# Kernel tuning notes

Measured on AMD Instinct MI355X. Metric: run time of the kernel, lower is better.

The kernel has to match this reference:

```python
import jax, jax.numpy as jnp
import numpy as np

B, C, R, Cc = 16384, 30, 7, 7

def setup_inputs() -> dict:
    key = jax.random.key(0)
    k1, k2, k3 = jax.random.split(key, 3)
    pred = jax.random.uniform(k1, (B, C, R, Cc), dtype=jnp.float32)
    label = jax.random.uniform(k2, (B, C, R, Cc), dtype=jnp.float32)
    obj = (jax.random.uniform(k3, (B, R, Cc)) > 0.7).astype(jnp.float32)
    label = label.at[:, 4].set(obj)
    return {"pred": pred, "label": label}

def _boxes(t, cols, rows, nrow, ncol, off):
    # t: [b,30,r,c]; channels off..off+3 are (x,y,w,h) relative to cell
    x, y, w, h = t[:, off], t[:, off + 1], t[:, off + 2], t[:, off + 3]
    cx = (x + cols) / ncol
    cy = (y + rows) / nrow
    return cx - w / 2, cy - h / 2, cx + w / 2, cy + h / 2

def _iou(a, b):
    ax1, ay1, ax2, ay2 = a
    bx1, by1, bx2, by2 = b
    iw = jnp.maximum(jnp.minimum(ax2, bx2) - jnp.maximum(ax1, bx1), 0.0)
    ih = jnp.maximum(jnp.minimum(ay2, by2) - jnp.maximum(ay1, by1), 0.0)
    inter = iw * ih
    area_a = (ax2 - ax1) * (ay2 - ay1)
    area_b = (bx2 - bx1) * (by2 - by1)
    return inter / (area_a + area_b - inter + 1e-10)

def reference(pred, label):
    b_size = pred.shape[0]
    nrow, ncol = pred.shape[-2], pred.shape[-1]
    cols = jnp.arange(ncol, dtype=pred.dtype)[None, None, :]  # [1,1,c]
    rows = jnp.arange(nrow, dtype=pred.dtype)[None, :, None]  # [1,r,1]

    bbox1 = _boxes(pred, cols, rows, nrow, ncol, 0)
    bbox2 = _boxes(pred, cols, rows, nrow, ncol, 5)
    lbox = _boxes(label, cols, rows, nrow, ncol, 0)
    iou1 = _iou(bbox1, lbox)  # [b,r,c]
    iou2 = _iou(bbox2, lbox)
    choose1 = iou1 >= iou2

    # coord loss candidates (sum over the 2 xy channels / 2 wh channels)
    coord1 = 5.0 * jnp.sum((pred[:, 0:2] - label[:, 0:2]) ** 2, axis=1) \
           + jnp.sum((jnp.sqrt(pred[:, 2:4]) - jnp.sqrt(label[:, 2:4])) ** 2, axis=1)
    coord2 = 5.0 * jnp.sum((pred[:, 5:7] - label[:, 5:7]) ** 2, axis=1) \
           + jnp.sum((jnp.sqrt(pred[:, 7:9]) - jnp.sqrt(label[:, 7:9])) ** 2, axis=1)

    obj1 = (pred[:, 4] - iou1) ** 2
    obj2 = (pred[:, 9] - iou2) ** 2

    coord = jnp.where(choose1, coord1, coord2)
    obj_conf = jnp.where(choose1, obj1, obj2)
    noobj_conf_obj = 0.5 * jnp.where(choose1, obj2, obj1)
    class_l = jnp.sum((pred[:, 10:] - label[:, 10:]) ** 2, axis=1)

    obj_cell = coord + obj_conf + noobj_conf_obj + class_l
    # note: original sums the two confidences THEN squares (faithful to source)
    noobj_cell = 0.5 * (pred[:, 4] + pred[:, 9]) ** 2

    is_obj = label[:, 4] == 1.0
    per_cell = jnp.where(is_obj, obj_cell, noobj_cell)
    return jnp.sum(per_cell) / b_size
```

## Files before the change

### kernel.cpp

```cpp
#include <hip/hip_runtime.h>


typedef float v2f __attribute__((ext_vector_type(2)));

#define NBATCH 16384
#define RECF 1470
#define BLOCK 256
#define GRID 2048
#define NWAVES (GRID * 4)

__device__ __forceinline__ float sq(float x) { return x * x; }

__device__ __forceinline__ float block_reduce(float v, float* smem, int tid) {
#pragma unroll
    for (int off = 32; off > 0; off >>= 1) v += __shfl_down(v, off, 64);
    const int lane = tid & 63, wave = tid >> 6;
    if (lane == 0) smem[wave] = v;
    __syncthreads();
    return smem[0] + smem[1] + smem[2] + smem[3];
}

__global__ __launch_bounds__(BLOCK) void k_class(const float* __restrict__ pred,
                                                 const float* __restrict__ label,
                                                 float* __restrict__ partials) {
    __shared__ float smem[4];
    const int tid = threadIdx.x, lane = tid & 63, wv = tid >> 6;
    const int gw = blockIdx.x * 4 + wv;
    const int c0 = (2 * lane) % 49;
    float acc = 0.0f;

    for (int rec = gw; rec < NBATCH; rec += NWAVES) {
        const float* rp = pred + (size_t)rec * RECF;
        const float* rl = label + (size_t)rec * RECF;
        float w49 = (lane < 49) ? rl[196 + lane] : 0.0f;
        int c = c0;
#pragma unroll
        for (int it = 0; it < 8; ++it) {
            int k = it * 64 + lane;
            v2f p2 = {0.0f, 0.0f}, l2 = {0.0f, 0.0f};
            if (k < 490) {
                p2 = __builtin_nontemporal_load((const v2f*)(rp + 490 + 2 * k));
                l2 = __builtin_nontemporal_load((const v2f*)(rl + 490 + 2 * k));
            }
            float w0 = __shfl(w49, c, 64);
            int cn = (c == 48) ? 0 : c + 1;
            float w1 = __shfl(w49, cn, 64);
            float d0 = p2.x - l2.x, d1 = p2.y - l2.y;
            acc += w0 * d0 * d0 + w1 * d1 * d1;
            c += 30; if (c >= 49) c -= 49;
        }
    }

    float s = block_reduce(acc, smem, tid);
    if (tid == 0) partials[blockIdx.x] = s;
}

__global__ __launch_bounds__(BLOCK) void k_box(const float* __restrict__ pred,
                                               const float* __restrict__ label,
                                               float* __restrict__ partials) {
    __shared__ float lds[4][960];
    __shared__ float smem[4];
    const int tid = threadIdx.x, lane = tid & 63, wv = tid >> 6;
    const int gw = blockIdx.x * 4 + wv;
    float* ldsw = &lds[wv][0];
    v2f* wp2 = (v2f*)ldsw;
    v2f* wl2 = (v2f*)(ldsw + 496);

    const int rr = lane / 7, cc = lane - rr * 7;
    const float fr = (float)rr, fcl = (float)cc;
    const float inv7 = 1.0f / 7.0f;
    float acc = 0.0f;

    for (int rec = gw; rec < NBATCH; rec += NWAVES) {
        const v2f* gp = (const v2f*)(pred + (size_t)rec * RECF);
        const v2f* gl = (const v2f*)(label + (size_t)rec * RECF);
#pragma unroll
        for (int r4 = 0; r4 < 4; ++r4) {
            int idx = r4 * 64 + lane;
            if (idx < 245) wp2[idx] = __builtin_nontemporal_load(gp + idx);
            if (idx < 221) wl2[idx] = __builtin_nontemporal_load(gl + idx);
        }
        asm volatile("s_waitcnt lgkmcnt(0)" ::: "memory");

        if (lane < 49) {
            float p[10], l[9];
#pragma unroll
            for (int ch = 0; ch < 10; ++ch) p[ch] = ldsw[ch * 49 + lane];
#pragma unroll
            for (int ch = 0; ch < 9; ++ch) l[ch] = ldsw[496 + ch * 49 + lane];

            float lcx = (l[0] + fcl) * inv7;
            float lcy = (l[1] + fr) * inv7;
            float lhw = l[2] * 0.5f, lhh = l[3] * 0.5f;
            float lx1 = lcx - lhw, ly1 = lcy - lhh;
            float lx2 = lcx + lhw, ly2 = lcy + lhh;
            float larea = (lx2 - lx1) * (ly2 - ly1);

            float cx1 = (p[0] + fcl) * inv7, cy1 = (p[1] + fr) * inv7;
            float x11 = cx1 - p[2] * 0.5f, y11 = cy1 - p[3] * 0.5f;
            float x12 = cx1 + p[2] * 0.5f, y12 = cy1 + p[3] * 0.5f;
            float iw1 = fmaxf(fminf(x12, lx2) - fmaxf(x11, lx1), 0.0f);
            float ih1 = fmaxf(fminf(y12, ly2) - fmaxf(y11, ly1), 0.0f);
            float int1 = iw1 * ih1;
            float a1 = (x12 - x11) * (y12 - y11);
            float iou1 = int1 / (a1 + larea - int1 + 1e-10f);

            float cx2 = (p[5] + fcl) * inv7, cy2 = (p[6] + fr) * inv7;
            float x21 = cx2 - p[7] * 0.5f, y21 = cy2 - p[8] * 0.5f;
            float x22 = cx2 + p[7] * 0.5f, y22 = cy2 + p[8] * 0.5f;
            float iw2 = fmaxf(fminf(x22, lx2) - fmaxf(x21, lx1), 0.0f);
            float ih2 = fmaxf(fminf(y22, ly2) - fmaxf(y21, ly1), 0.0f);
            float int2 = iw2 * ih2;
            float a2 = (x22 - x21) * (y22 - y21);
            float iou2 = int2 / (a2 + larea - int2 + 1e-10f);

            bool ch1 = iou1 >= iou2;

            float coord1 = 5.0f * (sq(p[0] - l[0]) + sq(p[1] - l[1]))
                         + sq(sqrtf(p[2]) - sqrtf(l[2])) + sq(sqrtf(p[3]) - sqrtf(l[3]));
            float coord2 = 5.0f * (sq(p[5] - l[5]) + sq(p[6] - l[6]))
                         + sq(sqrtf(p[7]) - sqrtf(l[7])) + sq(sqrtf(p[8]) - sqrtf(l[8]));
            float obj1 = sq(p[4] - iou1);
            float obj2 = sq(p[9] - iou2);

            float obj_cell = (ch1 ? coord1 : coord2)
                           + (ch1 ? obj1 : obj2)
                           + 0.5f * (ch1 ? obj2 : obj1);
            float noobj_cell = 0.5f * sq(p[4] + p[9]);

            acc += (l[4] == 1.0f) ? obj_cell : noobj_cell;
        }
    }

    float s = block_reduce(acc, smem, tid);
    if (tid == 0) partials[blockIdx.x] = s;
}

__global__ __launch_bounds__(BLOCK) void k_reduce(const float* __restrict__ partials,
                                                  float* __restrict__ out) {
    __shared__ float smem[4];
    float s = 0.0f;
#pragma unroll
    for (int it = 0; it < 2 * GRID / BLOCK; ++it)
        s += partials[it * BLOCK + threadIdx.x];
    float t = block_reduce(s, smem, threadIdx.x);
    if (threadIdx.x == 0) out[0] = t * (1.0f / (float)NBATCH);
}

extern "C" void kernel_launch(void* const* d_in, const int* in_sizes, int n_in,
                              void* d_out, int out_size, void* d_ws, size_t ws_size,
                              hipStream_t stream) {
    const float* pred  = (const float*)d_in[0];
    const float* label = (const float*)d_in[1];
    float* out = (float*)d_out;
    float* part1 = (float*)d_ws;
    float* part2 = part1 + GRID;

    k_class<<<GRID, BLOCK, 0, stream>>>(pred, label, part1);
    k_box<<<GRID, BLOCK, 0, stream>>>(pred, label, part2);
    k_reduce<<<1, BLOCK, 0, stream>>>(part1, out);
}
```

Baseline: 203.3 us.

## Fuse class and box kernels into one wave-per-record kernel

Merges the class-loss kernel and the box/IoU kernel into one kernel where each wave handles exactly one record. All global loads for the record are issued up front into registers, then the box channels are staged to LDS while the class loss is computed. This removes one kernel launch and the grid-stride loops, and lets both parts overlap their memory traffic. In exchange it raises register pressure from holding 24 vector loads per lane, launches many more blocks, and drops the nontemporal load hints.

```diff
diff --git a/kernel.cpp b/kernel.cpp
--- a/kernel.cpp
+++ b/kernel.cpp
@@ -6,8 +6,7 @@
 #define NBATCH 16384
 #define RECF 1470
 #define BLOCK 256
-#define GRID 2048
-#define NWAVES (GRID * 4)
+#define GRID (NBATCH / 4)
 
 __device__ __forceinline__ float sq(float x) { return x * x; }
 
@@ -20,116 +19,112 @@
     return smem[0] + smem[1] + smem[2] + smem[3];
 }
 
-__global__ __launch_bounds__(BLOCK) void k_class(const float* __restrict__ pred,
+__global__ __launch_bounds__(BLOCK) void k_fused(const float* __restrict__ pred,
                                                  const float* __restrict__ label,
                                                  float* __restrict__ partials) {
-    __shared__ float smem[4];
-    const int tid = threadIdx.x, lane = tid & 63, wv = tid >> 6;
-    const int gw = blockIdx.x * 4 + wv;
-    const int c0 = (2 * lane) % 49;
-    float acc = 0.0f;
-
-    for (int rec = gw; rec < NBATCH; rec += NWAVES) {
-        const float* rp = pred + (size_t)rec * RECF;
-        const float* rl = label + (size_t)rec * RECF;
-        float w49 = (lane < 49) ? rl[196 + lane] : 0.0f;
-        int c = c0;
-#pragma unroll
-        for (int it = 0; it < 8; ++it) {
-            int k = it * 64 + lane;
-            v2f p2 = {0.0f, 0.0f}, l2 = {0.0f, 0.0f};
-            if (k < 490) {
-                p2 = __builtin_nontemporal_load((const v2f*)(rp + 490 + 2 * k));
-                l2 = __builtin_nontemporal_load((const v2f*)(rl + 490 + 2 * k));
-            }
-            float w0 = __shfl(w49, c, 64);
-            int cn = (c == 48) ? 0 : c + 1;
-            float w1 = __shfl(w49, cn, 64);
-            float d0 = p2.x - l2.x, d1 = p2.y - l2.y;
-            acc += w0 * d0 * d0 + w1 * d1 * d1;
-            c += 30; if (c >= 49) c -= 49;
-        }
-    }
-
-    float s = block_reduce(acc, smem, tid);
-    if (tid == 0) partials[blockIdx.x] = s;
-}
-
-__global__ __launch_bounds__(BLOCK) void k_box(const float* __restrict__ pred,
-                                               const float* __restrict__ label,
-                                               float* __restrict__ partials) {
     __shared__ float lds[4][960];
     __shared__ float smem[4];
     const int tid = threadIdx.x, lane = tid & 63, wv = tid >> 6;
-    const int gw = blockIdx.x * 4 + wv;
+    const int rec = blockIdx.x * 4 + wv;
     float* ldsw = &lds[wv][0];
     v2f* wp2 = (v2f*)ldsw;
     v2f* wl2 = (v2f*)(ldsw + 496);
 
-    const int rr = lane / 7, cc = lane - rr * 7;
-    const float fr = (float)rr, fcl = (float)cc;
-    const float inv7 = 1.0f / 7.0f;
+    const v2f* gp = (const v2f*)(pred + (size_t)rec * RECF);
+    const v2f* gl = (const v2f*)(label + (size_t)rec * RECF);
+
+    v2f sp[4], sl[4];
+#pragma unroll
+    for (int i = 0; i < 4; ++i) {
+        int idx = i * 64 + lane;
+        sp[i] = (idx < 245) ? gp[idx] : (v2f){0.0f, 0.0f};
+        sl[i] = (idx < 221) ? gl[idx] : (v2f){0.0f, 0.0f};
+    }
+    v2f cpv[8], clv[8];
+#pragma unroll
+    for (int i = 0; i < 8; ++i) {
+        int k = i * 64 + lane;
+        if (k < 490) {
+            cpv[i] = gp[245 + k];
+            clv[i] = gl[245 + k];
+        } else {
+            cpv[i] = (v2f){0.0f, 0.0f};
+            clv[i] = (v2f){0.0f, 0.0f};
+        }
+    }
+    float w49 = (lane < 49) ? ((const float*)gl)[196 + lane] : 0.0f;
+
+#pragma unroll
+    for (int i = 0; i < 4; ++i) {
+        int idx = i * 64 + lane;
+        if (idx < 245) wp2[idx] = sp[i];
+        if (idx < 221) wl2[idx] = sl[i];
+    }
+
     float acc = 0.0f;
+    int c = (2 * lane) % 49;
+#pragma unroll
+    for (int i = 0; i < 8; ++i) {
+        float w0 = __shfl(w49, c, 64);
+        int cn = (c == 48) ? 0 : c + 1;
+        float w1 = __shfl(w49, cn, 64);
+        float d0 = cpv[i].x - clv[i].x, d1 = cpv[i].y - clv[i].y;
+        acc += w0 * d0 * d0 + w1 * d1 * d1;
+        c += 30; if (c >= 49) c -= 49;
+    }
 
-    for (int rec = gw; rec < NBATCH; rec += NWAVES) {
-        const v2f* gp = (const v2f*)(pred + (size_t)rec * RECF);
-        const v2f* gl = (const v2f*)(label + (size_t)rec * RECF);
+    asm volatile("s_waitcnt lgkmcnt(0)" ::: "memory");
+    if (lane < 49) {
+        const int rr = lane / 7, cc = lane - rr * 7;
+        const float fr = (float)rr, fcl = (float)cc;
+        const float inv7 = 1.0f / 7.0f;
+
+        float p[10], l[9];
 #pragma unroll
-        for (int r4 = 0; r4 < 4; ++r4) {
-            int idx = r4 * 64 + lane;
-            if (idx < 245) wp2[idx] = __builtin_nontemporal_load(gp + idx);
-            if (idx < 221) wl2[idx] = __builtin_nontemporal_load(gl + idx);
-        }
-        asm volatile("s_waitcnt lgkmcnt(0)" ::: "memory");
+        for (int ch = 0; ch < 10; ++ch) p[ch] = ldsw[ch * 49 + lane];
+#pragma unroll
+        for (int ch = 0; ch < 9; ++ch) l[ch] = ldsw[496 + ch * 49 + lane];
 
-        if (lane < 49) {
-            float p[10], l[9];
-#pragma unroll
-            for (int ch = 0; ch < 10; ++ch) p[ch] = ldsw[ch * 49 + lane];
-#pragma unroll
-            for (int ch = 0; ch < 9; ++ch) l[ch] = ldsw[496 + ch * 49 + lane];
+        float lcx = (l[0] + fcl) * inv7;
+        float lcy = (l[1] + fr) * inv7;
+        float lhw = l[2] * 0.5f, lhh = l[3] * 0.5f;
+        float lx1 = lcx - lhw, ly1 = lcy - lhh;
+        float lx2 = lcx + lhw, ly2 = lcy + lhh;
+        float larea = (lx2 - lx1) * (ly2 - ly1);
 
-            float lcx = (l[0] + fcl) * inv7;
-            float lcy = (l[1] + fr) * inv7;
-            float lhw = l[2] * 0.5f, lhh = l[3] * 0.5f;
-            float lx1 = lcx - lhw, ly1 = lcy - lhh;
-            float lx2 = lcx + lhw, ly2 = lcy + lhh;
-            float larea = (lx2 - lx1) * (ly2 - ly1);
+        float cx1 = (p[0] + fcl) * inv7, cy1 = (p[1] + fr) * inv7;
+        float x11 = cx1 - p[2] * 0.5f, y11 = cy1 - p[3] * 0.5f;
+        float x12 = cx1 + p[2] * 0.5f, y12 = cy1 + p[3] * 0.5f;
+        float iw1 = fmaxf(fminf(x12, lx2) - fmaxf(x11, lx1), 0.0f);
+        float ih1 = fmaxf(fminf(y12, ly2) - fmaxf(y11, ly1), 0.0f);
+        float int1 = iw1 * ih1;
+        float a1 = (x12 - x11) * (y12 - y11);
+        float iou1 = int1 / (a1 + larea - int1 + 1e-10f);
 
-            float cx1 = (p[0] + fcl) * inv7, cy1 = (p[1] + fr) * inv7;
-            float x11 = cx1 - p[2] * 0.5f, y11 = cy1 - p[3] * 0.5f;
-            float x12 = cx1 + p[2] * 0.5f, y12 = cy1 + p[3] * 0.5f;
-            float iw1 = fmaxf(fminf(x12, lx2) - fmaxf(x11, lx1), 0.0f);
-            float ih1 = fmaxf(fminf(y12, ly2) - fmaxf(y11, ly1), 0.0f);
-            float int1 = iw1 * ih1;
-            float a1 = (x12 - x11) * (y12 - y11);
-            float iou1 = int1 / (a1 + larea - int1 + 1e-10f);
+        float cx2 = (p[5] + fcl) * inv7, cy2 = (p[6] + fr) * inv7;
+        float x21 = cx2 - p[7] * 0.5f, y21 = cy2 - p[8] * 0.5f;
+        float x22 = cx2 + p[7] * 0.5f, y22 = cy2 + p[8] * 0.5f;
+        float iw2 = fmaxf(fminf(x22, lx2) - fmaxf(x21, lx1), 0.0f);
+        float ih2 = fmaxf(fminf(y22, ly2) - fmaxf(y21, ly1), 0.0f);
+        float int2 = iw2 * ih2;
+        float a2 = (x22 - x21) * (y22 - y21);
+        float iou2 = int2 / (a2 + larea - int2 + 1e-10f);
 
-            float cx2 = (p[5] + fcl) * inv7, cy2 = (p[6] + fr) * inv7;
-            float x21 = cx2 - p[7] * 0.5f, y21 = cy2 - p[8] * 0.5f;
-            float x22 = cx2 + p[7] * 0.5f, y22 = cy2 + p[8] * 0.5f;
-            float iw2 = fmaxf(fminf(x22, lx2) - fmaxf(x21, lx1), 0.0f);
-            float ih2 = fmaxf(fminf(y22, ly2) - fmaxf(y21, ly1), 0.0f);
-            float int2 = iw2 * ih2;
-            float a2 = (x22 - x21) * (y22 - y21);
-            float iou2 = int2 / (a2 + larea - int2 + 1e-10f);
+        bool ch1 = iou1 >= iou2;
 
-            bool ch1 = iou1 >= iou2;
+        float coord1 = 5.0f * (sq(p[0] - l[0]) + sq(p[1] - l[1]))
+                     + sq(sqrtf(p[2]) - sqrtf(l[2])) + sq(sqrtf(p[3]) - sqrtf(l[3]));
+        float coord2 = 5.0f * (sq(p[5] - l[5]) + sq(p[6] - l[6]))
+                     + sq(sqrtf(p[7]) - sqrtf(l[7])) + sq(sqrtf(p[8]) - sqrtf(l[8]));
+        float obj1 = sq(p[4] - iou1);
+        float obj2 = sq(p[9] - iou2);
 
-            float coord1 = 5.0f * (sq(p[0] - l[0]) + sq(p[1] - l[1]))
-                         + sq(sqrtf(p[2]) - sqrtf(l[2])) + sq(sqrtf(p[3]) - sqrtf(l[3]));
-            float coord2 = 5.0f * (sq(p[5] - l[5]) + sq(p[6] - l[6]))
-                         + sq(sqrtf(p[7]) - sqrtf(l[7])) + sq(sqrtf(p[8]) - sqrtf(l[8]));
-            float obj1 = sq(p[4] - iou1);
-            float obj2 = sq(p[9] - iou2);
+        float obj_cell = (ch1 ? coord1 : coord2)
+                       + (ch1 ? obj1 : obj2)
+                       + 0.5f * (ch1 ? obj2 : obj1);
+        float noobj_cell = 0.5f * sq(p[4] + p[9]);
 
-            float obj_cell = (ch1 ? coord1 : coord2)
-                           + (ch1 ? obj1 : obj2)
-                           + 0.5f * (ch1 ? obj2 : obj1);
-            float noobj_cell = 0.5f * sq(p[4] + p[9]);
-
-            acc += (l[4] == 1.0f) ? obj_cell : noobj_cell;
-        }
+        acc += (l[4] == 1.0f) ? obj_cell : noobj_cell;
     }
 
     float s = block_reduce(acc, smem, tid);
@@ -141,7 +136,7 @@
     __shared__ float smem[4];
     float s = 0.0f;
 #pragma unroll
-    for (int it = 0; it < 2 * GRID / BLOCK; ++it)
+    for (int it = 0; it < GRID / BLOCK; ++it)
         s += partials[it * BLOCK + threadIdx.x];
     float t = block_reduce(s, smem, threadIdx.x);
     if (threadIdx.x == 0) out[0] = t * (1.0f / (float)NBATCH);
@@ -153,10 +148,8 @@
     const float* pred  = (const float*)d_in[0];
     const float* label = (const float*)d_in[1];
     float* out = (float*)d_out;
-    float* part1 = (float*)d_ws;
-    float* part2 = part1 + GRID;
+    float* part = (float*)d_ws;
 
-    k_class<<<GRID, BLOCK, 0, stream>>>(pred, label, part1);
-    k_box<<<GRID, BLOCK, 0, stream>>>(pred, label, part2);
-    k_reduce<<<1, BLOCK, 0, stream>>>(part1, out);
+    k_fused<<<GRID, BLOCK, 0, stream>>>(pred, label, part);
+    k_reduce<<<1, BLOCK, 0, stream>>>(part, out);
 }
```

After: 204.3 us. About the same (+0.5%).
